# Kernel optimization log

Hardware: AMD Instinct MI355X
Metric: run time of the kernel (lower is better)

## Reference

```python
import jax, jax.numpy as jnp
import numpy as np

B, N, K, H, NC, NL = 512, 128, 16, 16, 6, 4  # batch, atoms, neighbors/atom, h_a, classes, EGNN layers

def _lin(key, fi, fo):
    lim = 1.0 / np.sqrt(fi)
    return jax.random.uniform(key, (fi, fo), jnp.float32, -lim, lim)

def _bias(key, fi, fo):
    lim = 1.0 / np.sqrt(fi)
    return jax.random.uniform(key, (fo,), jnp.float32, -lim, lim)

def setup_inputs():
    key = jax.random.key(0)
    kc, ke, ki, ko, kf, kl = jax.random.split(key, 6)
    coords = jax.random.normal(kc, (B, N, 3), dtype=jnp.float32)
    # fixed adjacency: node i -> (i+1 .. i+K) mod N, same for every frame
    adj = np.zeros((N, N), dtype=np.float32)
    idx = np.arange(N)
    for d in range(1, K + 1):
        adj[idx, (idx + d) % N] = 1.0
    data = jnp.concatenate([coords, jnp.broadcast_to(jnp.asarray(adj), (B, N, N))], axis=-1)  # [B,N,3+N]
    # edge-index construction (host-side; matches torch (edge_inds>0).nonzero().t(), row/col += offset*N)
    off, r, c = np.nonzero(np.broadcast_to(adj > 0.0, (B, N, N)))
    row = jnp.asarray(r + off * N, dtype=jnp.int32)
    col = jnp.asarray(c + off * N, dtype=jnp.int32)
    emb_w = jax.random.normal(ke, (N, H), dtype=jnp.float32)  # atom_emb.weight.data.normal_()
    k1, k2 = jax.random.split(ki); ein_w, ein_b = _lin(k1, H, H), _bias(k2, H, H)
    k1, k2 = jax.random.split(ko); eout_w, eout_b = _lin(k1, H, H), _bias(k2, H, H)
    k1, k2 = jax.random.split(kf); fc_w, fc_b = _lin(k1, H, NC), _bias(k2, H, NC)
    def make_layer(k):
        ks = jax.random.split(k, 11)
        xav = 0.001 * np.sqrt(6.0 / (H + 1))  # coord_mlp last layer: xavier_uniform gain=0.001, no bias
        return dict(
            e1_w=_lin(ks[0], 2 * H + 2, H), e1_b=_bias(ks[1], 2 * H + 2, H),
            e2_w=_lin(ks[2], H, H),        e2_b=_bias(ks[3], H, H),
            n1_w=_lin(ks[4], 2 * H, H),    n1_b=_bias(ks[5], 2 * H, H),
            n2_w=_lin(ks[6], H, H),        n2_b=_bias(ks[7], H, H),
            c1_w=_lin(ks[8], H, H),        c1_b=_bias(ks[9], H, H),
            c2_w=jax.random.uniform(ks[10], (H, 1), jnp.float32, -xav, xav))
    layers = [make_layer(k) for k in jax.random.split(kl, NL)]
    stacked = {name: jnp.stack([l[name] for l in layers]) for name in layers[0]}  # [NL, ...]
    out = dict(data=data, row=row, col=col, emb_w=emb_w, ein_w=ein_w, ein_b=ein_b,
               eout_w=eout_w, eout_b=eout_b, fc_w=fc_w, fc_b=fc_b)
    out.update(stacked)
    return out

def reference(data, row, col, emb_w, ein_w, ein_b, eout_w, eout_b, fc_w, fc_b,
              e1_w, e1_b, e2_w, e2_b, n1_w, n1_b, n2_w, n2_b, c1_w, c1_b, c2_w):
    Bn = data.shape[0] * data.shape[1]  # B*N flattened nodes
    silu = jax.nn.silu
    seg = lambda v: jax.ops.segment_sum(v, row, num_segments=Bn)
    # atom_emb(arange(N)) repeated over batch -> tile embedding table rows
    h = jnp.broadcast_to(emb_w[None, :, :], (data.shape[0], data.shape[1], H)).reshape(Bn, H)
    x = data[:, :, :3].reshape(Bn, 3).astype(jnp.float32)
    e_attr = jnp.ones((row.shape[0], 1), jnp.float32)
    cnt = jnp.maximum(seg(jnp.ones((row.shape[0],), jnp.float32)), 1.0)[:, None]  # for coords_agg='mean'
    h = h @ ein_w + ein_b  # embedding_in
    for l in range(NL):  # E_GCL layers (residual=True, attention=False)
        cd = x[row] - x[col]                                  # [E,3] coord_diff
        radial = jnp.sum(cd * cd, axis=1, keepdims=True)      # [E,1]
        ein = jnp.concatenate([h[row], h[col], radial, e_attr], axis=1)  # [E, 2H+2]
        m = silu(silu(ein @ e1_w[l] + e1_b[l]) @ e2_w[l] + e2_b[l])      # edge_mlp -> [E,H]
        t = silu(m @ c1_w[l] + c1_b[l]) @ c2_w[l]             # coord_mlp -> [E,1]
        x = x + seg(cd * t) / cnt                             # mean-aggregated coord update
        agg_m = seg(m)                                        # scatter-add messages to nodes
        h = h + (silu(jnp.concatenate([h, agg_m], axis=1) @ n1_w[l] + n1_b[l]) @ n2_w[l] + n2_b[l])
    h = h @ eout_w + eout_b  # embedding_out
    prot = jnp.sum(h.reshape(data.shape[0], data.shape[1], H), axis=1) / N  # pooling
    return jax.nn.softmax(prot @ fc_w + fc_b, axis=-1)
```

## Files before the change

### kernel.cpp

```cpp
#include <hip/hip_runtime.h>
#include <math.h>


#define NB   512
#define NN   128
#define HH   16
#define NCLS 6
#define NLAY 4
#define PAD  20

#define W_E1   0
#define W_E1B  544
#define W_E2   560
#define W_E2B  816
#define W_C1   832
#define W_C1B  1088
#define W_C2   1104
#define W_N1   1120
#define W_N1B  1632
#define W_N2   1648
#define W_N2B  1904
#define W_TOT  1920

typedef float f32x2 __attribute__((ext_vector_type(2)));

__device__ __forceinline__ float silu_f(float v) {
    return __fdividef(v, 1.f + __expf(-v));
}
__device__ __forceinline__ f32x2 mk2(float x, float y) { f32x2 r; r.x = x; r.y = y; return r; }
__device__ __forceinline__ f32x2 splat2(float x)       { f32x2 r; r.x = x; r.y = x; return r; }
__device__ __forceinline__ f32x2 lo2(float4 v)         { return mk2(v.x, v.y); }
__device__ __forceinline__ f32x2 hi2(float4 v)         { return mk2(v.z, v.w); }
__device__ __forceinline__ f32x2 silu2(f32x2 v) {
    f32x2 r; r.x = silu_f(v.x); r.y = silu_f(v.y); return r;
}

extern "C" __global__ __launch_bounds__(512, 2)
void GraphVampNet_73624329388105_kernel(
    const float* __restrict__ data,
    const float* __restrict__ emb_w,
    const float* __restrict__ ein_w, const float* __restrict__ ein_b,
    const float* __restrict__ eout_w, const float* __restrict__ eout_b,
    const float* __restrict__ fc_w,  const float* __restrict__ fc_b,
    const float* __restrict__ e1_w,  const float* __restrict__ e1_b,
    const float* __restrict__ e2_w,  const float* __restrict__ e2_b,
    const float* __restrict__ n1_w,  const float* __restrict__ n1_b,
    const float* __restrict__ n2_w,  const float* __restrict__ n2_b,
    const float* __restrict__ c1_w,  const float* __restrict__ c1_b,
    const float* __restrict__ c2_w,
    float* __restrict__ out)
{
    __shared__ float h[NN][PAD];
    __shared__ float xs[NN][4];
    __shared__ float pA[NN][PAD];
    __shared__ float pB[NN][PAD];
    __shared__ float part[3 * NN][PAD];
    __shared__ __align__(16) float wb[W_TOT];
    __shared__ float hp[HH];
    __shared__ float prot[HH];

    const int b = blockIdx.x;
    const int t = threadIdx.x;

    if (t < NN) {
        const float* dp = data + ((size_t)b * NN + t) * (NN + 3);
        xs[t][0] = dp[0]; xs[t][1] = dp[1]; xs[t][2] = dp[2]; xs[t][3] = 0.f;

        float ev[HH];
        #pragma unroll
        for (int k = 0; k < HH; k++) ev[k] = emb_w[t * HH + k];
        float acc[HH];
        #pragma unroll
        for (int o = 0; o < HH; o++) acc[o] = ein_b[o];
        #pragma unroll
        for (int k = 0; k < HH; k++) {
            const float v = ev[k];
            #pragma unroll
            for (int o = 0; o < HH; o++) acc[o] += v * ein_w[k * HH + o];
        }
        #pragma unroll
        for (int o = 0; o < HH; o++) h[t][o] = acc[o];
    }

    #pragma unroll 1
    for (int l = 0; l < NLAY; l++) {
        {
            const float* E1W = e1_w + l * 34 * HH;
            wb[W_E1 + t] = E1W[t];
            if (t < 32) wb[W_E1 + 512 + t] = E1W[512 + t];
            const float* N1W = n1_w + l * 2 * HH * HH;
            wb[W_N1 + t] = N1W[t];
            if (t < 256) {
                wb[W_E2 + t] = e2_w[l * HH * HH + t];
                wb[W_C1 + t] = c1_w[l * HH * HH + t];
                wb[W_N2 + t] = n2_w[l * HH * HH + t];
            }
            if (t < HH) {
                wb[W_E1B + t] = e1_b[l * HH + t];
                wb[W_E2B + t] = e2_b[l * HH + t];
                wb[W_C1B + t] = c1_b[l * HH + t];
                wb[W_C2  + t] = c2_w[l * HH + t];
                wb[W_N1B + t] = n1_b[l * HH + t];
                wb[W_N2B + t] = n2_b[l * HH + t];
            }
        }
        __syncthreads();

        {
            const int node = t & (NN - 1);
            const int grp = t >> 7;
            const int ob = (grp & 1) * 8;
            float hv[HH];
            #pragma unroll
            for (int k = 0; k < HH; k++) hv[k] = h[node][k];
            if (grp < 2) {
                float acc[8];
                #pragma unroll
                for (int o = 0; o < 8; o++)
                    acc[o] = wb[W_E1B + ob + o] + wb[W_E1 + 33 * HH + ob + o];
                #pragma unroll
                for (int k = 0; k < HH; k++) {
                    const float v = hv[k];
                    #pragma unroll
                    for (int o = 0; o < 8; o++) acc[o] += v * wb[W_E1 + k * HH + ob + o];
                }
                #pragma unroll
                for (int o = 0; o < 8; o++) pA[node][ob + o] = acc[o];
            } else {
                float acc[8];
                #pragma unroll
                for (int o = 0; o < 8; o++) acc[o] = 0.f;
                #pragma unroll
                for (int k = 0; k < HH; k++) {
                    const float v = hv[k];
                    #pragma unroll
                    for (int o = 0; o < 8; o++) acc[o] += v * wb[W_E1 + (16 + k) * HH + ob + o];
                }
                #pragma unroll
                for (int o = 0; o < 8; o++) pB[node][ob + o] = acc[o];
            }
        }
        __syncthreads();

        float aggm[HH];
        float cx0 = 0.f, cx1 = 0.f, cx2 = 0.f;
        {
            const int i = t & (NN - 1);
            const int q4 = t >> 7;
            const float4 xi = *(const float4*)&xs[i][0];
            #pragma unroll
            for (int o = 0; o < HH; o++) aggm[o] = 0.f;

            #pragma unroll 1
            for (int g = 0; g < 2; g++) {
                unsigned o0 = 0;
                asm volatile("" : "+v"(o0));
                const float* wbl = (const float*)wb + o0;

                const int dbase = q4 * 4 + g * 2 + 1;
                const int j0 = (i + dbase) & (NN - 1);
                const int j1 = (i + dbase + 1) & (NN - 1);
                const float4 xj0 = *(const float4*)&xs[j0][0];
                const float4 xj1 = *(const float4*)&xs[j1][0];
                const float a00 = xi.x - xj0.x, a01 = xi.y - xj0.y, a02 = xi.z - xj0.z;
                const float a10 = xi.x - xj1.x, a11 = xi.y - xj1.y, a12 = xi.z - xj1.z;
                const float r0 = a00 * a00 + a01 * a01 + a02 * a02;
                const float r1 = a10 * a10 + a11 * a11 + a12 * a12;
                const f32x2 r0s = splat2(r0), r1s = splat2(r1);

                f32x2 m0[8], m1[8];
                #pragma unroll
                for (int q = 0; q < 4; q++) {
                    const float4 wc = ((const float4*)(wbl + W_E1 + 32 * HH))[q];
                    const float4 pa = *(const float4*)&pA[i][q * 4];
                    const float4 p0 = *(const float4*)&pB[j0][q * 4];
                    const float4 p1 = *(const float4*)&pB[j1][q * 4];
                    const f32x2 palo = lo2(pa), pahi = hi2(pa);
                    const f32x2 wclo = lo2(wc), wchi = hi2(wc);
                    m0[q*2+0] = silu2(palo + lo2(p0) + r0s * wclo);
                    m0[q*2+1] = silu2(pahi + hi2(p0) + r0s * wchi);
                    m1[q*2+0] = silu2(palo + lo2(p1) + r1s * wclo);
                    m1[q*2+1] = silu2(pahi + hi2(p1) + r1s * wchi);
                }

                f32x2 ca0[8], ca1[8];
                #pragma unroll
                for (int q = 0; q < 4; q++) {
                    const float4 bb = ((const float4*)(wbl + W_C1B))[q];
                    ca0[q*2+0] = lo2(bb); ca0[q*2+1] = hi2(bb);
                    ca1[q*2+0] = lo2(bb); ca1[q*2+1] = hi2(bb);
                }

                #pragma unroll
                for (int hf = 0; hf < 2; hf++) {
                    f32x2 ac0[4], ac1[4];
                    #pragma unroll
                    for (int q = 0; q < 2; q++) {
                        const float4 bb = ((const float4*)(wbl + W_E2B))[hf * 2 + q];
                        ac0[q*2+0] = lo2(bb); ac0[q*2+1] = hi2(bb);
                        ac1[q*2+0] = lo2(bb); ac1[q*2+1] = hi2(bb);
                    }
                    #pragma unroll
                    for (int k = 0; k < HH; k++) {
                        const float e0  = (k & 1) ? m0[k >> 1].y : m0[k >> 1].x;
                        const float e1v = (k & 1) ? m1[k >> 1].y : m1[k >> 1].x;
                        const f32x2 v0 = splat2(e0), v1 = splat2(e1v);
                        #pragma unroll
                        for (int q = 0; q < 2; q++) {
                            const float4 w = ((const float4*)(wbl + W_E2))[k * 4 + hf * 2 + q];
                            ac0[q*2+0] += v0 * lo2(w); ac0[q*2+1] += v0 * hi2(w);
                            ac1[q*2+0] += v1 * lo2(w); ac1[q*2+1] += v1 * hi2(w);
                        }
                    }
                    #pragma unroll
                    for (int o = 0; o < 8; o++) {
                        const float s0 = silu_f((o & 1) ? ac0[o >> 1].y : ac0[o >> 1].x);
                        const float s1 = silu_f((o & 1) ? ac1[o >> 1].y : ac1[o >> 1].x);
                        const int kk = hf * 8 + o;
                        aggm[kk] += s0 + s1;
                        const f32x2 s0d = splat2(s0), s1d = splat2(s1);
                        #pragma unroll
                        for (int q = 0; q < 4; q++) {
                            const float4 w = ((const float4*)(wbl + W_C1))[kk * 4 + q];
                            ca0[q*2+0] += s0d * lo2(w); ca0[q*2+1] += s0d * hi2(w);
                            ca1[q*2+0] += s1d * lo2(w); ca1[q*2+1] += s1d * hi2(w);
                        }
                    }
                }

                f32x2 t0a = splat2(0.f), t1a = splat2(0.f);
                #pragma unroll
                for (int q = 0; q < 4; q++) {
                    const float4 cw = ((const float4*)(wbl + W_C2))[q];
                    t0a += silu2(ca0[q*2+0]) * lo2(cw);
                    t0a += silu2(ca0[q*2+1]) * hi2(cw);
                    t1a += silu2(ca1[q*2+0]) * lo2(cw);
                    t1a += silu2(ca1[q*2+1]) * hi2(cw);
                }
                const float t0 = t0a.x + t0a.y;
                const float t1 = t1a.x + t1a.y;

                cx0 += a00 * t0 + a10 * t1;
                cx1 += a01 * t0 + a11 * t1;
                cx2 += a02 * t0 + a12 * t1;
            }
            if (t >= NN) {
                #pragma unroll
                for (int o = 0; o < HH; o++) part[t - NN][o] = aggm[o];
                float4 cxv; cxv.x = cx0; cxv.y = cx1; cxv.z = cx2; cxv.w = 0.f;
                *(float4*)&part[t - NN][16] = cxv;
            }
        }
        __syncthreads();

        if (t < NN) {
            float am[HH];
            #pragma unroll
            for (int o = 0; o < HH; o++)
                am[o] = aggm[o] + part[t][o] + part[t + NN][o] + part[t + 2 * NN][o];
            float hv[HH];
            #pragma unroll
            for (int k = 0; k < HH; k++) hv[k] = h[t][k];

            float acc[HH];
            #pragma unroll
            for (int o = 0; o < HH; o++) acc[o] = wb[W_N1B + o];
            #pragma unroll
            for (int k = 0; k < HH; k++) {
                const float v = hv[k];
                #pragma unroll
                for (int o = 0; o < HH; o++) acc[o] += v * wb[W_N1 + k * HH + o];
            }
            #pragma unroll
            for (int k = 0; k < HH; k++) {
                const float v = am[k];
                #pragma unroll
                for (int o = 0; o < HH; o++) acc[o] += v * wb[W_N1 + (16 + k) * HH + o];
            }
            float u[HH];
            #pragma unroll
            for (int o = 0; o < HH; o++) u[o] = silu_f(acc[o]);

            float acc2[HH];
            #pragma unroll
            for (int o = 0; o < HH; o++) acc2[o] = wb[W_N2B + o];
            #pragma unroll
            for (int k = 0; k < HH; k++) {
                const float v = u[k];
                #pragma unroll
                for (int o = 0; o < HH; o++) acc2[o] += v * wb[W_N2 + k * HH + o];
            }
            #pragma unroll
            for (int o = 0; o < HH; o++) h[t][o] = hv[o] + acc2[o];

            const float inv = 1.f / 16.f;
            xs[t][0] += (cx0 + part[t][16] + part[t + NN][16] + part[t + 2 * NN][16]) * inv;
            xs[t][1] += (cx1 + part[t][17] + part[t + NN][17] + part[t + 2 * NN][17]) * inv;
            xs[t][2] += (cx2 + part[t][18] + part[t + NN][18] + part[t + 2 * NN][18]) * inv;
        }
        __syncthreads();
    }

    if (t < HH) {
        float acc = 0.f;
        for (int i = 0; i < NN; i++) acc += h[i][t];
        hp[t] = acc * (1.f / NN);
    }
    __syncthreads();
    if (t < HH) {
        float acc = eout_b[t];
        #pragma unroll
        for (int k = 0; k < HH; k++) acc += hp[k] * eout_w[k * HH + t];
        prot[t] = acc;
    }
    __syncthreads();
    if (t == 0) {
        float lg[NCLS];
        float mx = -1e30f;
        #pragma unroll
        for (int c = 0; c < NCLS; c++) {
            float acc = fc_b[c];
            #pragma unroll
            for (int k = 0; k < HH; k++) acc += prot[k] * fc_w[k * NCLS + c];
            lg[c] = acc;
            mx = fmaxf(mx, acc);
        }
        float s = 0.f;
        #pragma unroll
        for (int c = 0; c < NCLS; c++) { lg[c] = __expf(lg[c] - mx); s += lg[c]; }
        const float invs = 1.f / s;
        #pragma unroll
        for (int c = 0; c < NCLS; c++) out[b * NCLS + c] = lg[c] * invs;
    }
}

extern "C" void kernel_launch(void* const* d_in, const int* in_sizes, int n_in,
                              void* d_out, int out_size, void* d_ws, size_t ws_size,
                              hipStream_t stream) {
    const float* data   = (const float*)d_in[0];
    const float* emb_w  = (const float*)d_in[3];
    const float* ein_w  = (const float*)d_in[4];
    const float* ein_b  = (const float*)d_in[5];
    const float* eout_w = (const float*)d_in[6];
    const float* eout_b = (const float*)d_in[7];
    const float* fc_w   = (const float*)d_in[8];
    const float* fc_b   = (const float*)d_in[9];
    const float* e1_w   = (const float*)d_in[10];
    const float* e1_b   = (const float*)d_in[11];
    const float* e2_w   = (const float*)d_in[12];
    const float* e2_b   = (const float*)d_in[13];
    const float* n1_w   = (const float*)d_in[14];
    const float* n1_b   = (const float*)d_in[15];
    const float* n2_w   = (const float*)d_in[16];
    const float* n2_b   = (const float*)d_in[17];
    const float* c1_w   = (const float*)d_in[18];
    const float* c1_b   = (const float*)d_in[19];
    const float* c2_w   = (const float*)d_in[20];

    GraphVampNet_73624329388105_kernel<<<NB, 512, 0, stream>>>(
        data, emb_w, ein_w, ein_b, eout_w, eout_b, fc_w, fc_b,
        e1_w, e1_b, e2_w, e2_b, n1_w, n1_b, n2_w, n2_b, c1_w, c1_b, c2_w,
        (float*)d_out);
}
```

Measured before the change: 323.7 us.

## Parallelize node MLP across all threads and reduce edge partials with LDS atomics

Instead of only 128 of 512 threads doing the node MLP after a partial-sum buffer, edge partials are now accumulated with shared-memory atomicAdd into a zeroed accumulator. The node MLP is then split across four thread groups, each computing four output channels with packed float2 math, with an extra barrier and the hidden activations staged through LDS. silu2 uses a hardware reciprocal. This removes idle threads in the serial node stage, at the cost of LDS atomics, an additional barrier, and changed summation order.

```diff
diff --git a/kernel.cpp b/kernel.cpp
--- a/kernel.cpp
+++ b/kernel.cpp
@@ -32,7 +32,10 @@
 __device__ __forceinline__ f32x2 lo2(float4 v)         { return mk2(v.x, v.y); }
 __device__ __forceinline__ f32x2 hi2(float4 v)         { return mk2(v.z, v.w); }
 __device__ __forceinline__ f32x2 silu2(f32x2 v) {
-    f32x2 r; r.x = silu_f(v.x); r.y = silu_f(v.y); return r;
+    f32x2 e; e.x = __expf(-v.x); e.y = __expf(-v.y);
+    const f32x2 den = splat2(1.f) + e;
+    f32x2 r; r.x = __builtin_amdgcn_rcpf(den.x); r.y = __builtin_amdgcn_rcpf(den.y);
+    return v * r;
 }
 
 extern "C" __global__ __launch_bounds__(512, 2)
@@ -54,7 +57,7 @@
     __shared__ float xs[NN][4];
     __shared__ float pA[NN][PAD];
     __shared__ float pB[NN][PAD];
-    __shared__ float part[3 * NN][PAD];
+    __shared__ float accs[NN][PAD];
     __shared__ __align__(16) float wb[W_TOT];
     __shared__ float hp[HH];
     __shared__ float prot[HH];
@@ -103,6 +106,14 @@
                 wb[W_N1B + t] = n1_b[l * HH + t];
                 wb[W_N2B + t] = n2_b[l * HH + t];
             }
+            if (t < NN) {
+                float4 z; z.x = 0.f; z.y = 0.f; z.z = 0.f; z.w = 0.f;
+                *(float4*)&accs[t][0]  = z;
+                *(float4*)&accs[t][4]  = z;
+                *(float4*)&accs[t][8]  = z;
+                *(float4*)&accs[t][12] = z;
+                *(float4*)&accs[t][16] = z;
+            }
         }
         __syncthreads();
 
@@ -142,12 +153,12 @@
         }
         __syncthreads();
 
-        float aggm[HH];
-        float cx0 = 0.f, cx1 = 0.f, cx2 = 0.f;
         {
             const int i = t & (NN - 1);
             const int q4 = t >> 7;
             const float4 xi = *(const float4*)&xs[i][0];
+            float aggm[HH];
+            float cx0 = 0.f, cx1 = 0.f, cx2 = 0.f;
             #pragma unroll
             for (int o = 0; o < HH; o++) aggm[o] = 0.f;
 
@@ -244,59 +255,71 @@
                 cx1 += a01 * t0 + a11 * t1;
                 cx2 += a02 * t0 + a12 * t1;
             }
-            if (t >= NN) {
-                #pragma unroll
-                for (int o = 0; o < HH; o++) part[t - NN][o] = aggm[o];
-                float4 cxv; cxv.x = cx0; cxv.y = cx1; cxv.z = cx2; cxv.w = 0.f;
-                *(float4*)&part[t - NN][16] = cxv;
-            }
-        }
-        __syncthreads();
-
-        if (t < NN) {
-            float am[HH];
-            #pragma unroll
-            for (int o = 0; o < HH; o++)
-                am[o] = aggm[o] + part[t][o] + part[t + NN][o] + part[t + 2 * NN][o];
-            float hv[HH];
-            #pragma unroll
-            for (int k = 0; k < HH; k++) hv[k] = h[t][k];
-
-            float acc[HH];
-            #pragma unroll
-            for (int o = 0; o < HH; o++) acc[o] = wb[W_N1B + o];
+            #pragma unroll
+            for (int o = 0; o < HH; o++) atomicAdd(&accs[i][o], aggm[o]);
+            atomicAdd(&accs[i][16], cx0);
+            atomicAdd(&accs[i][17], cx1);
+            atomicAdd(&accs[i][18], cx2);
+        }
+        __syncthreads();
+
+        {
+            const int n = t & (NN - 1);
+            const int q = t >> 7;
+            float am[HH], hv[HH];
+            #pragma unroll
+            for (int qq = 0; qq < 4; qq++) {
+                const float4 a = *(const float4*)&accs[n][qq * 4];
+                am[qq*4+0] = a.x; am[qq*4+1] = a.y; am[qq*4+2] = a.z; am[qq*4+3] = a.w;
+                const float4 hh4 = *(const float4*)&h[n][qq * 4];
+                hv[qq*4+0] = hh4.x; hv[qq*4+1] = hh4.y; hv[qq*4+2] = hh4.z; hv[qq*4+3] = hh4.w;
+            }
+            const float4 bb = ((const float4*)(wb + W_N1B))[q];
+            f32x2 aA = lo2(bb), aB = hi2(bb);
             #pragma unroll
             for (int k = 0; k < HH; k++) {
-                const float v = hv[k];
-                #pragma unroll
-                for (int o = 0; o < HH; o++) acc[o] += v * wb[W_N1 + k * HH + o];
+                const float4 w = ((const float4*)(wb + W_N1))[k * 4 + q];
+                const f32x2 v = splat2(hv[k]);
+                aA += v * lo2(w); aB += v * hi2(w);
             }
             #pragma unroll
             for (int k = 0; k < HH; k++) {
-                const float v = am[k];
-                #pragma unroll
-                for (int o = 0; o < HH; o++) acc[o] += v * wb[W_N1 + (16 + k) * HH + o];
-            }
+                const float4 w = ((const float4*)(wb + W_N1))[(16 + k) * 4 + q];
+                const f32x2 v = splat2(am[k]);
+                aA += v * lo2(w); aB += v * hi2(w);
+            }
+            const f32x2 uA = silu2(aA), uB = silu2(aB);
+            float4 uq; uq.x = uA.x; uq.y = uA.y; uq.z = uB.x; uq.w = uB.y;
+            *(float4*)&pB[n][q * 4] = uq;
+        }
+        __syncthreads();
+        {
+            const int n = t & (NN - 1);
+            const int q = t >> 7;
             float u[HH];
             #pragma unroll
-            for (int o = 0; o < HH; o++) u[o] = silu_f(acc[o]);
-
-            float acc2[HH];
-            #pragma unroll
-            for (int o = 0; o < HH; o++) acc2[o] = wb[W_N2B + o];
+            for (int qq = 0; qq < 4; qq++) {
+                const float4 uu = *(const float4*)&pB[n][qq * 4];
+                u[qq*4+0] = uu.x; u[qq*4+1] = uu.y; u[qq*4+2] = uu.z; u[qq*4+3] = uu.w;
+            }
+            const float4 bb = ((const float4*)(wb + W_N2B))[q];
+            f32x2 aA = lo2(bb), aB = hi2(bb);
             #pragma unroll
             for (int k = 0; k < HH; k++) {
-                const float v = u[k];
-                #pragma unroll
-                for (int o = 0; o < HH; o++) acc2[o] += v * wb[W_N2 + k * HH + o];
-            }
-            #pragma unroll
-            for (int o = 0; o < HH; o++) h[t][o] = hv[o] + acc2[o];
-
-            const float inv = 1.f / 16.f;
-            xs[t][0] += (cx0 + part[t][16] + part[t + NN][16] + part[t + 2 * NN][16]) * inv;
-            xs[t][1] += (cx1 + part[t][17] + part[t + NN][17] + part[t + 2 * NN][17]) * inv;
-            xs[t][2] += (cx2 + part[t][18] + part[t + NN][18] + part[t + 2 * NN][18]) * inv;
+                const float4 w = ((const float4*)(wb + W_N2))[k * 4 + q];
+                const f32x2 v = splat2(u[k]);
+                aA += v * lo2(w); aB += v * hi2(w);
+            }
+            float4 hq = *(const float4*)&h[n][q * 4];
+            hq.x += aA.x; hq.y += aA.y; hq.z += aB.x; hq.w += aB.y;
+            *(float4*)&h[n][q * 4] = hq;
+
+            if (t < NN) {
+                const float inv = 1.f / 16.f;
+                xs[t][0] += accs[t][16] * inv;
+                xs[t][1] += accs[t][17] * inv;
+                xs[t][2] += accs[t][18] * inv;
+            }
         }
         __syncthreads();
     }
```

Result: slower. 336.1 us (+3.8%).

## Read edge/coord MLP weights as uniform scalar loads from a prepacked workspace

Applied to the files above, without the earlier changes.

A small prep kernel repacks e2_w and c1_w into a column-chunked layout in a workspace. The main kernel now reads those weights, plus the e1 radial column, e2/c1 biases and c2 weights, straight from global memory through wave-uniform pointers, so they can become scalar (SGPR) loads instead of LDS reads. The edge and coord MLPs are restructured to process output columns in groups of four, loading 16-float weight blocks at once. This aims to remove LDS bandwidth pressure in the hot edge loop, at the cost of an extra kernel launch and higher SGPR use.

```diff
diff --git a/kernel.cpp b/kernel.cpp
--- a/kernel.cpp
+++ b/kernel.cpp
@@ -11,18 +11,14 @@
 
 #define W_E1   0
 #define W_E1B  544
-#define W_E2   560
-#define W_E2B  816
-#define W_C1   832
-#define W_C1B  1088
-#define W_C2   1104
-#define W_N1   1120
-#define W_N1B  1632
-#define W_N2   1648
-#define W_N2B  1904
-#define W_TOT  1920
+#define W_N1   560
+#define W_N1B  1072
+#define W_N2   1088
+#define W_N2B  1344
+#define W_TOT  1360
 
 typedef float f32x2 __attribute__((ext_vector_type(2)));
+struct __align__(64) f16B { float4 a, b, c, d; };
 
 __device__ __forceinline__ float silu_f(float v) {
     return __fdividef(v, 1.f + __expf(-v));
@@ -33,6 +29,20 @@
 __device__ __forceinline__ f32x2 hi2(float4 v)         { return mk2(v.z, v.w); }
 __device__ __forceinline__ f32x2 silu2(f32x2 v) {
     f32x2 r; r.x = silu_f(v.x); r.y = silu_f(v.y); return r;
+}
+
+__global__ void GraphVampNet_prep_kernel(const float* __restrict__ e2_w,
+                                         const float* __restrict__ c1_w,
+                                         float* __restrict__ ws) {
+    const int idx = blockIdx.x * 256 + threadIdx.x;
+    if (idx >= NLAY * 2 * 256) return;
+    const int j   = idx & 3;
+    const int k   = (idx >> 2) & 15;
+    const int c   = (idx >> 6) & 3;
+    const int mat = (idx >> 8) & 1;
+    const int l   = idx >> 9;
+    const float* src = mat ? c1_w : e2_w;
+    ws[idx] = src[l * 256 + k * 16 + c * 4 + j];
 }
 
 extern "C" __global__ __launch_bounds__(512, 2)
@@ -48,6 +58,7 @@
     const float* __restrict__ n2_w,  const float* __restrict__ n2_b,
     const float* __restrict__ c1_w,  const float* __restrict__ c1_b,
     const float* __restrict__ c2_w,
+    const float* __restrict__ ws,
     float* __restrict__ out)
 {
     __shared__ float h[NN][PAD];
@@ -90,16 +101,9 @@
             if (t < 32) wb[W_E1 + 512 + t] = E1W[512 + t];
             const float* N1W = n1_w + l * 2 * HH * HH;
             wb[W_N1 + t] = N1W[t];
-            if (t < 256) {
-                wb[W_E2 + t] = e2_w[l * HH * HH + t];
-                wb[W_C1 + t] = c1_w[l * HH * HH + t];
-                wb[W_N2 + t] = n2_w[l * HH * HH + t];
-            }
+            if (t < 256) wb[W_N2 + t] = n2_w[l * HH * HH + t];
             if (t < HH) {
                 wb[W_E1B + t] = e1_b[l * HH + t];
-                wb[W_E2B + t] = e2_b[l * HH + t];
-                wb[W_C1B + t] = c1_b[l * HH + t];
-                wb[W_C2  + t] = c2_w[l * HH + t];
                 wb[W_N1B + t] = n1_b[l * HH + t];
                 wb[W_N2B + t] = n2_b[l * HH + t];
             }
@@ -151,11 +155,20 @@
             #pragma unroll
             for (int o = 0; o < HH; o++) aggm[o] = 0.f;
 
+            const float* wsE2 = ws + (size_t)(l * 2) * 256;
+            const float* wsC1 = ws + (size_t)(l * 2 + 1) * 256;
+
             #pragma unroll 1
             for (int g = 0; g < 2; g++) {
                 unsigned o0 = 0;
                 asm volatile("" : "+v"(o0));
-                const float* wbl = (const float*)wb + o0;
+                const float* pAl = (const float*)pA + o0;
+                const float* pBl = (const float*)pB + o0;
+                const float* E1C  = e1_w + l * 34 * HH + 32 * HH;
+                const float* E2B_ = e2_b + l * HH;
+                const float* C1B_ = c1_b + l * HH;
+                const float* C2_  = c2_w + l * HH;
+                asm volatile("" : "+s"(E1C), "+s"(E2B_), "+s"(C1B_), "+s"(C2_));
 
                 const int dbase = q4 * 4 + g * 2 + 1;
                 const int j0 = (i + dbase) & (NN - 1);
@@ -171,10 +184,10 @@
                 f32x2 m0[8], m1[8];
                 #pragma unroll
                 for (int q = 0; q < 4; q++) {
-                    const float4 wc = ((const float4*)(wbl + W_E1 + 32 * HH))[q];
-                    const float4 pa = *(const float4*)&pA[i][q * 4];
-                    const float4 p0 = *(const float4*)&pB[j0][q * 4];
-                    const float4 p1 = *(const float4*)&pB[j1][q * 4];
+                    const float4 wc = ((const float4*)E1C)[q];
+                    const float4 pa = *(const float4*)(pAl + i * PAD + q * 4);
+                    const float4 p0 = *(const float4*)(pBl + j0 * PAD + q * 4);
+                    const float4 p1 = *(const float4*)(pBl + j1 * PAD + q * 4);
                     const f32x2 palo = lo2(pa), pahi = hi2(pa);
                     const f32x2 wclo = lo2(wc), wchi = hi2(wc);
                     m0[q*2+0] = silu2(palo + lo2(p0) + r0s * wclo);
@@ -183,60 +196,71 @@
                     m1[q*2+1] = silu2(pahi + hi2(p1) + r1s * wchi);
                 }
 
-                f32x2 ca0[8], ca1[8];
-                #pragma unroll
-                for (int q = 0; q < 4; q++) {
-                    const float4 bb = ((const float4*)(wbl + W_C1B))[q];
-                    ca0[q*2+0] = lo2(bb); ca0[q*2+1] = hi2(bb);
-                    ca1[q*2+0] = lo2(bb); ca1[q*2+1] = hi2(bb);
-                }
-
-                #pragma unroll
-                for (int hf = 0; hf < 2; hf++) {
-                    f32x2 ac0[4], ac1[4];
+                #define MGET(ARR, KI) ((KI & 1) ? ARR[KI >> 1].y : ARR[KI >> 1].x)
+
+                f32x2 mp0[8], mp1[8];
+                #pragma unroll
+                for (int c = 0; c < 4; c++) {
+                    const float4 bb = ((const float4*)E2B_)[c];
+                    f32x2 a0l = lo2(bb), a0h = hi2(bb);
+                    f32x2 a1l = lo2(bb), a1h = hi2(bb);
                     #pragma unroll
-                    for (int q = 0; q < 2; q++) {
-                        const float4 bb = ((const float4*)(wbl + W_E2B))[hf * 2 + q];
-                        ac0[q*2+0] = lo2(bb); ac0[q*2+1] = hi2(bb);
-                        ac1[q*2+0] = lo2(bb); ac1[q*2+1] = hi2(bb);
+                    for (int hg = 0; hg < 2; hg++) {
+                        const float* wph = wsE2 + c * 64 + hg * 32;
+                        asm volatile("" : "+s"(wph));
+                        const f16B W0 = *(const f16B*)(wph);
+                        const f16B W1 = *(const f16B*)(wph + 16);
+                        #define E2STEP(WROW, KI) { \
+                            const f32x2 v0 = splat2(MGET(m0, KI)); \
+                            const f32x2 v1 = splat2(MGET(m1, KI)); \
+                            a0l += v0 * lo2(WROW); a0h += v0 * hi2(WROW); \
+                            a1l += v1 * lo2(WROW); a1h += v1 * hi2(WROW); }
+                        E2STEP(W0.a, (hg * 8 + 0)) E2STEP(W0.b, (hg * 8 + 1))
+                        E2STEP(W0.c, (hg * 8 + 2)) E2STEP(W0.d, (hg * 8 + 3))
+                        E2STEP(W1.a, (hg * 8 + 4)) E2STEP(W1.b, (hg * 8 + 5))
+                        E2STEP(W1.c, (hg * 8 + 6)) E2STEP(W1.d, (hg * 8 + 7))
+                        #undef E2STEP
                     }
+                    const f32x2 s0l = silu2(a0l), s0h = silu2(a0h);
+                    const f32x2 s1l = silu2(a1l), s1h = silu2(a1h);
+                    mp0[c*2+0] = s0l; mp0[c*2+1] = s0h;
+                    mp1[c*2+0] = s1l; mp1[c*2+1] = s1h;
+                    aggm[c*4+0] += s0l.x + s1l.x;
+                    aggm[c*4+1] += s0l.y + s1l.y;
+                    aggm[c*4+2] += s0h.x + s1h.x;
+                    aggm[c*4+3] += s0h.y + s1h.y;
+                }
+
+                f32x2 t0a = splat2(0.f), t1a = splat2(0.f);
+                #pragma unroll
+                for (int c = 0; c < 4; c++) {
+                    const float4 bb = ((const float4*)C1B_)[c];
+                    f32x2 a0l = lo2(bb), a0h = hi2(bb);
+                    f32x2 a1l = lo2(bb), a1h = hi2(bb);
                     #pragma unroll
-                    for (int k = 0; k < HH; k++) {
-                        const float e0  = (k & 1) ? m0[k >> 1].y : m0[k >> 1].x;
-                        const float e1v = (k & 1) ? m1[k >> 1].y : m1[k >> 1].x;
-                        const f32x2 v0 = splat2(e0), v1 = splat2(e1v);
-                        #pragma unroll
-                        for (int q = 0; q < 2; q++) {
-                            const float4 w = ((const float4*)(wbl + W_E2))[k * 4 + hf * 2 + q];
-                            ac0[q*2+0] += v0 * lo2(w); ac0[q*2+1] += v0 * hi2(w);
-                            ac1[q*2+0] += v1 * lo2(w); ac1[q*2+1] += v1 * hi2(w);
-                        }
+                    for (int hg = 0; hg < 2; hg++) {
+                        const float* wph = wsC1 + c * 64 + hg * 32;
+                        asm volatile("" : "+s"(wph));
+                        const f16B W0 = *(const f16B*)(wph);
+                        const f16B W1 = *(const f16B*)(wph + 16);
+                        #define C1STEP(WROW, KI) { \
+                            const f32x2 v0 = splat2(MGET(mp0, KI)); \
+                            const f32x2 v1 = splat2(MGET(mp1, KI)); \
+                            a0l += v0 * lo2(WROW); a0h += v0 * hi2(WROW); \
+                            a1l += v1 * lo2(WROW); a1h += v1 * hi2(WROW); }
+                        C1STEP(W0.a, (hg * 8 + 0)) C1STEP(W0.b, (hg * 8 + 1))
+                        C1STEP(W0.c, (hg * 8 + 2)) C1STEP(W0.d, (hg * 8 + 3))
+                        C1STEP(W1.a, (hg * 8 + 4)) C1STEP(W1.b, (hg * 8 + 5))
+                        C1STEP(W1.c, (hg * 8 + 6)) C1STEP(W1.d, (hg * 8 + 7))
+                        #undef C1STEP
                     }
-                    #pragma unroll
-                    for (int o = 0; o < 8; o++) {
-                        const float s0 = silu_f((o & 1) ? ac0[o >> 1].y : ac0[o >> 1].x);
-                        const float s1 = silu_f((o & 1) ? ac1[o >> 1].y : ac1[o >> 1].x);
-                        const int kk = hf * 8 + o;
-                        aggm[kk] += s0 + s1;
-                        const f32x2 s0d = splat2(s0), s1d = splat2(s1);
-                        #pragma unroll
-                        for (int q = 0; q < 4; q++) {
-                            const float4 w = ((const float4*)(wbl + W_C1))[kk * 4 + q];
-                            ca0[q*2+0] += s0d * lo2(w); ca0[q*2+1] += s0d * hi2(w);
-                            ca1[q*2+0] += s1d * lo2(w); ca1[q*2+1] += s1d * hi2(w);
-                        }
-                    }
-                }
-
-                f32x2 t0a = splat2(0.f), t1a = splat2(0.f);
-                #pragma unroll
-                for (int q = 0; q < 4; q++) {
-                    const float4 cw = ((const float4*)(wbl + W_C2))[q];
-                    t0a += silu2(ca0[q*2+0]) * lo2(cw);
-                    t0a += silu2(ca0[q*2+1]) * hi2(cw);
-                    t1a += silu2(ca1[q*2+0]) * lo2(cw);
-                    t1a += silu2(ca1[q*2+1]) * hi2(cw);
-                }
+                    const float4 cw = ((const float4*)C2_)[c];
+                    t0a += silu2(a0l) * lo2(cw);
+                    t0a += silu2(a0h) * hi2(cw);
+                    t1a += silu2(a1l) * lo2(cw);
+                    t1a += silu2(a1h) * hi2(cw);
+                }
+                #undef MGET
                 const float t0 = t0a.x + t0a.y;
                 const float t1 = t1a.x + t1a.y;
 
@@ -356,9 +380,12 @@
     const float* c1_w   = (const float*)d_in[18];
     const float* c1_b   = (const float*)d_in[19];
     const float* c2_w   = (const float*)d_in[20];
+    float* ws = (float*)d_ws;
+
+    GraphVampNet_prep_kernel<<<8, 256, 0, stream>>>(e2_w, c1_w, ws);
 
     GraphVampNet_73624329388105_kernel<<<NB, 512, 0, stream>>>(
         data, emb_w, ein_w, ein_b, eout_w, eout_b, fc_w, fc_b,
         e1_w, e1_b, e2_w, e2_b, n1_w, n1_b, n2_w, n2_b, c1_w, c1_b, c2_w,
-        (float*)d_out);
-}
+        ws, (float*)d_out);
+}
```

Measured after the change: 553.1 us. 1.71x slower.

## Swizzle shared-memory node rows by rotating float4 chunks and split coords into SoA

Applied to the files above, without the earlier changes.

Node-feature arrays in shared memory (h, pA, pB, part) now place each row's float4 chunks in an order rotated by row mod 5, and node coordinates move from an AoS float4 array to three separate arrays. The goal is to reduce LDS bank conflicts on the strided float4 reads and writes that neighbour gathers and row accesses make with a 20-float pitch. In exchange, every access pays extra index arithmetic, including a modulo by 5 and conditional subtracts. Some previously scalar h accesses become float4.

```diff
diff --git a/kernel.cpp b/kernel.cpp
--- a/kernel.cpp
+++ b/kernel.cpp
@@ -33,6 +33,15 @@
 __device__ __forceinline__ f32x2 hi2(float4 v)         { return mk2(v.z, v.w); }
 __device__ __forceinline__ f32x2 silu2(f32x2 v) {
     f32x2 r; r.x = silu_f(v.x); r.y = silu_f(v.y); return r;
+}
+
+__device__ __forceinline__ int rot5(int r) { return r % 5; }
+__device__ __forceinline__ int qoff(int rot, int q) {
+    int s = q + rot;
+    return (s >= 5 ? s - 5 : s) * 4;
+}
+__device__ __forceinline__ int sidx(int row, int rot, int k) {
+    return row * PAD + qoff(rot, k >> 2) + (k & 3);
 }
 
 extern "C" __global__ __launch_bounds__(512, 2)
@@ -50,11 +59,11 @@
     const float* __restrict__ c2_w,
     float* __restrict__ out)
 {
-    __shared__ float h[NN][PAD];
-    __shared__ float xs[NN][4];
-    __shared__ float pA[NN][PAD];
-    __shared__ float pB[NN][PAD];
-    __shared__ float part[3 * NN][PAD];
+    __shared__ float h[NN * PAD];
+    __shared__ float xsx[NN], xsy[NN], xsz[NN];
+    __shared__ float pA[NN * PAD];
+    __shared__ float pB[NN * PAD];
+    __shared__ float part[3 * NN * PAD];
     __shared__ __align__(16) float wb[W_TOT];
     __shared__ float hp[HH];
     __shared__ float prot[HH];
@@ -64,7 +73,7 @@
 
     if (t < NN) {
         const float* dp = data + ((size_t)b * NN + t) * (NN + 3);
-        xs[t][0] = dp[0]; xs[t][1] = dp[1]; xs[t][2] = dp[2]; xs[t][3] = 0.f;
+        xsx[t] = dp[0]; xsy[t] = dp[1]; xsz[t] = dp[2];
 
         float ev[HH];
         #pragma unroll
@@ -78,8 +87,12 @@
             #pragma unroll
             for (int o = 0; o < HH; o++) acc[o] += v * ein_w[k * HH + o];
         }
-        #pragma unroll
-        for (int o = 0; o < HH; o++) h[t][o] = acc[o];
+        const int rt = rot5(t);
+        #pragma unroll
+        for (int q = 0; q < 4; q++) {
+            float4 v; v.x = acc[q*4+0]; v.y = acc[q*4+1]; v.z = acc[q*4+2]; v.w = acc[q*4+3];
+            *(float4*)&h[t * PAD + qoff(rt, q)] = v;
+        }
     }
 
     #pragma unroll 1
@@ -108,11 +121,12 @@
 
         {
             const int node = t & (NN - 1);
+            const int rn = rot5(node);
             const int grp = t >> 7;
             const int ob = (grp & 1) * 8;
             float hv[HH];
             #pragma unroll
-            for (int k = 0; k < HH; k++) hv[k] = h[node][k];
+            for (int k = 0; k < HH; k++) hv[k] = h[sidx(node, rn, k)];
             if (grp < 2) {
                 float acc[8];
                 #pragma unroll
@@ -125,7 +139,7 @@
                     for (int o = 0; o < 8; o++) acc[o] += v * wb[W_E1 + k * HH + ob + o];
                 }
                 #pragma unroll
-                for (int o = 0; o < 8; o++) pA[node][ob + o] = acc[o];
+                for (int o = 0; o < 8; o++) pA[sidx(node, rn, ob + o)] = acc[o];
             } else {
                 float acc[8];
                 #pragma unroll
@@ -137,7 +151,7 @@
                     for (int o = 0; o < 8; o++) acc[o] += v * wb[W_E1 + (16 + k) * HH + ob + o];
                 }
                 #pragma unroll
-                for (int o = 0; o < 8; o++) pB[node][ob + o] = acc[o];
+                for (int o = 0; o < 8; o++) pB[sidx(node, rn, ob + o)] = acc[o];
             }
         }
         __syncthreads();
@@ -147,7 +161,8 @@
         {
             const int i = t & (NN - 1);
             const int q4 = t >> 7;
-            const float4 xi = *(const float4*)&xs[i][0];
+            const int ri = rot5(i);
+            const float xix = xsx[i], xiy = xsy[i], xiz = xsz[i];
             #pragma unroll
             for (int o = 0; o < HH; o++) aggm[o] = 0.f;
 
@@ -160,10 +175,9 @@
                 const int dbase = q4 * 4 + g * 2 + 1;
                 const int j0 = (i + dbase) & (NN - 1);
                 const int j1 = (i + dbase + 1) & (NN - 1);
-                const float4 xj0 = *(const float4*)&xs[j0][0];
-                const float4 xj1 = *(const float4*)&xs[j1][0];
-                const float a00 = xi.x - xj0.x, a01 = xi.y - xj0.y, a02 = xi.z - xj0.z;
-                const float a10 = xi.x - xj1.x, a11 = xi.y - xj1.y, a12 = xi.z - xj1.z;
+                const int rj0 = rot5(j0), rj1 = rot5(j1);
+                const float a00 = xix - xsx[j0], a01 = xiy - xsy[j0], a02 = xiz - xsz[j0];
+                const float a10 = xix - xsx[j1], a11 = xiy - xsy[j1], a12 = xiz - xsz[j1];
                 const float r0 = a00 * a00 + a01 * a01 + a02 * a02;
                 const float r1 = a10 * a10 + a11 * a11 + a12 * a12;
                 const f32x2 r0s = splat2(r0), r1s = splat2(r1);
@@ -172,9 +186,9 @@
                 #pragma unroll
                 for (int q = 0; q < 4; q++) {
                     const float4 wc = ((const float4*)(wbl + W_E1 + 32 * HH))[q];
-                    const float4 pa = *(const float4*)&pA[i][q * 4];
-                    const float4 p0 = *(const float4*)&pB[j0][q * 4];
-                    const float4 p1 = *(const float4*)&pB[j1][q * 4];
+                    const float4 pa = *(const float4*)&pA[i * PAD + qoff(ri, q)];
+                    const float4 p0 = *(const float4*)&pB[j0 * PAD + qoff(rj0, q)];
+                    const float4 p1 = *(const float4*)&pB[j1 * PAD + qoff(rj1, q)];
                     const f32x2 palo = lo2(pa), pahi = hi2(pa);
                     const f32x2 wclo = lo2(wc), wchi = hi2(wc);
                     m0[q*2+0] = silu2(palo + lo2(p0) + r0s * wclo);
@@ -245,22 +259,44 @@
                 cx2 += a02 * t0 + a12 * t1;
             }
             if (t >= NN) {
-                #pragma unroll
-                for (int o = 0; o < HH; o++) part[t - NN][o] = aggm[o];
+                const int row = t - NN;
+                const int rp = rot5(row);
+                #pragma unroll
+                for (int q = 0; q < 4; q++) {
+                    float4 v; v.x = aggm[q*4+0]; v.y = aggm[q*4+1];
+                    v.z = aggm[q*4+2]; v.w = aggm[q*4+3];
+                    *(float4*)&part[row * PAD + qoff(rp, q)] = v;
+                }
                 float4 cxv; cxv.x = cx0; cxv.y = cx1; cxv.z = cx2; cxv.w = 0.f;
-                *(float4*)&part[t - NN][16] = cxv;
+                *(float4*)&part[row * PAD + qoff(rp, 4)] = cxv;
             }
         }
         __syncthreads();
 
         if (t < NN) {
+            const int rt = rot5(t);
             float am[HH];
             #pragma unroll
-            for (int o = 0; o < HH; o++)
-                am[o] = aggm[o] + part[t][o] + part[t + NN][o] + part[t + 2 * NN][o];
+            for (int o = 0; o < HH; o++) am[o] = aggm[o];
+            float pc0 = cx0, pc1 = cx1, pc2 = cx2;
+            #pragma unroll
+            for (int s = 0; s < 3; s++) {
+                const int row = t + s * NN;
+                const int rp = rot5(row);
+                #pragma unroll
+                for (int q = 0; q < 4; q++) {
+                    const float4 v = *(const float4*)&part[row * PAD + qoff(rp, q)];
+                    am[q*4+0] += v.x; am[q*4+1] += v.y; am[q*4+2] += v.z; am[q*4+3] += v.w;
+                }
+                const float4 cxv = *(const float4*)&part[row * PAD + qoff(rp, 4)];
+                pc0 += cxv.x; pc1 += cxv.y; pc2 += cxv.z;
+            }
             float hv[HH];
             #pragma unroll
-            for (int k = 0; k < HH; k++) hv[k] = h[t][k];
+            for (int q = 0; q < 4; q++) {
+                const float4 v = *(const float4*)&h[t * PAD + qoff(rt, q)];
+                hv[q*4+0] = v.x; hv[q*4+1] = v.y; hv[q*4+2] = v.z; hv[q*4+3] = v.w;
+            }
 
             float acc[HH];
             #pragma unroll
@@ -291,19 +327,24 @@
                 for (int o = 0; o < HH; o++) acc2[o] += v * wb[W_N2 + k * HH + o];
             }
             #pragma unroll
-            for (int o = 0; o < HH; o++) h[t][o] = hv[o] + acc2[o];
+            for (int q = 0; q < 4; q++) {
+                float4 v;
+                v.x = hv[q*4+0] + acc2[q*4+0]; v.y = hv[q*4+1] + acc2[q*4+1];
+                v.z = hv[q*4+2] + acc2[q*4+2]; v.w = hv[q*4+3] + acc2[q*4+3];
+                *(float4*)&h[t * PAD + qoff(rt, q)] = v;
+            }
 
             const float inv = 1.f / 16.f;
-            xs[t][0] += (cx0 + part[t][16] + part[t + NN][16] + part[t + 2 * NN][16]) * inv;
-            xs[t][1] += (cx1 + part[t][17] + part[t + NN][17] + part[t + 2 * NN][17]) * inv;
-            xs[t][2] += (cx2 + part[t][18] + part[t + NN][18] + part[t + 2 * NN][18]) * inv;
+            xsx[t] += pc0 * inv;
+            xsy[t] += pc1 * inv;
+            xsz[t] += pc2 * inv;
         }
         __syncthreads();
     }
 
     if (t < HH) {
         float acc = 0.f;
-        for (int i = 0; i < NN; i++) acc += h[i][t];
+        for (int i = 0; i < NN; i++) acc += h[sidx(i, rot5(i), t)];
         hp[t] = acc * (1.f / NN);
     }
     __syncthreads();
```

New measurement: 377.5 us. 1.17x slower.
